# Optimization experiments

Measured on AMD Instinct MI355X. Metric: run time of the kernel, lower is better.

Reference implementation:

```python
import jax, jax.numpy as jnp
import numpy as np

B, L, H, NH, E, M, P, NL, BLK = 4, 1024, 768, 12, 24, 4, 552, 97, 64
NEG = -1e30

def setup_inputs() -> dict:
    key = jax.random.key(0)
    ks = jax.random.split(key, 10)
    sequence_output = jax.random.normal(ks[0], (B, L, H), jnp.float32)
    attention = jax.nn.softmax(jax.random.normal(ks[1], (B, NH, L, L), jnp.float32), axis=-1)
    mention_idx = jax.random.randint(ks[2], (B, E, M), 0, L)
    # first mention of each entity always valid, rest random (ragged mention counts)
    mention_mask = jnp.concatenate(
        [jnp.ones((B, E, 1), jnp.float32),
         (jax.random.uniform(ks[3], (B, E, M - 1)) > 0.4).astype(jnp.float32)], axis=-1)
    hts = jax.random.randint(ks[4], (B, P, 2), 0, E)
    s = 0.02
    Wh = jax.random.normal(ks[5], (H, 2 * H), jnp.float32) * s
    bh = jnp.zeros((H,), jnp.float32)
    Wt = jax.random.normal(ks[6], (H, 2 * H), jnp.float32) * s
    bt = jnp.zeros((H,), jnp.float32)
    Wb = jax.random.normal(ks[7], (NL, H * BLK), jnp.float32) * s
    bb = jnp.zeros((NL,), jnp.float32)
    return {"sequence_output": sequence_output, "attention": attention,
            "mention_mask": mention_mask, "Wh": Wh, "bh": bh, "Wt": Wt, "bt": bt,
            "Wb": Wb, "bb": bb, "mention_idx": mention_idx, "hts": hts}

def reference(sequence_output, attention, mention_mask, Wh, bh, Wt, bt, Wb, bb, mention_idx, hts):
    bix = jnp.arange(B)[:, None, None]
    # gather mention embeddings: [B,E,M,H]
    m_emb = sequence_output[bix, mention_idx]
    mask = mention_mask[..., None]
    # entity embedding: logsumexp over valid mentions
    entity_embs = jax.nn.logsumexp(jnp.where(mask > 0, m_emb, NEG), axis=2)  # [B,E,H]
    # gather mention attention rows: [B,E,M,NH,L]; mean over valid mentions
    m_att = attention[bix, :, mention_idx]
    denom = jnp.sum(mention_mask, axis=-1)[:, :, None, None]
    entity_atts = jnp.sum(m_att * mask[..., None], axis=2) / denom  # [B,E,NH,L]
    b2 = jnp.arange(B)[:, None]
    hs = entity_embs[b2, hts[..., 0]]   # [B,P,H]
    ts = entity_embs[b2, hts[..., 1]]
    h_att = entity_atts[b2, hts[..., 0]]  # [B,P,NH,L]
    t_att = entity_atts[b2, hts[..., 1]]
    ht_att = (h_att * t_att).mean(axis=2)                     # [B,P,L]
    ht_att = ht_att / (ht_att.sum(-1, keepdims=True) + 1e-5)
    rs = jnp.einsum('bld,brl->brd', sequence_output, ht_att)  # [B,P,H]
    zh = jnp.tanh(jnp.concatenate([hs, rs], -1) @ Wh.T + bh)  # [B,P,H]
    zt = jnp.tanh(jnp.concatenate([ts, rs], -1) @ Wt.T + bt)
    b1 = zh.reshape(B, P, H // BLK, BLK)
    b2_ = zt.reshape(B, P, H // BLK, BLK)
    bl = (b1[..., :, None] * b2_[..., None, :]).reshape(B, P, H * BLK)
    logits = bl @ Wb.T + bb                                   # [B,P,NL]
    return logits
```

## Files before the change

### kernel.cpp

```cpp
#include <hip/hip_runtime.h>
#include <math.h>

#define B_   4
#define L_   1024
#define H_   768
#define NH_  12
#define E_   24
#define M_   4
#define P_   552
#define NL_  97
#define H2_  1536
#define HB_  49152
#define R_   2208
#define NEG_ (-1e30f)

#define RT2_  9
#define PR2_  2304
#define S_    24
#define NTIL_ 7
#define KT_   1536

typedef _Float16 h2   __attribute__((ext_vector_type(2)));
typedef _Float16 f16x8 __attribute__((ext_vector_type(8)));
typedef float    f32x4 __attribute__((ext_vector_type(4)));

__device__ inline uint pkh(float lo, float hi) {
    union { __fp16 v __attribute__((ext_vector_type(2))); uint u; } c;
    c.v = __builtin_amdgcn_cvt_pkrtz(lo, hi);
    return c.u;
}
__device__ inline ushort h_rne(float x) {
    union { _Float16 h; ushort u; } c; c.h = (_Float16)x; return c.u;
}
__device__ inline uint h2_rne(float lo, float hi) {
    return (uint)h_rne(lo) | ((uint)h_rne(hi) << 16);
}

#define PKB_ATT 1152
#define PKB_WB  2688
#define PKB_W   576
#define PKB_SEQ 1536
#define PKB_EMB 96
__global__ void k_pack(const float* __restrict__ att, const float* __restrict__ Wb,
                       const float* __restrict__ Wh, const float* __restrict__ Wt,
                       const float* __restrict__ seq,
                       const int* __restrict__ midx, const float* __restrict__ mmask,
                       _Float16* __restrict__ ea, _Float16* __restrict__ WbP,
                       _Float16* __restrict__ WhP, _Float16* __restrict__ WtP,
                       _Float16* __restrict__ seqP, _Float16* __restrict__ ee) {
    int bid = blockIdx.x;
    if (bid < PKB_ATT) {
        int blk = bid;
        int n  = blk % NH_;
        int be = blk / NH_;
        int b  = be / E_;
        int idx[M_]; float msk[M_]; float denom = 0.f;
#pragma unroll
        for (int m = 0; m < M_; ++m) { idx[m] = midx[be*M_+m]; msk[m] = mmask[be*M_+m]; denom += msk[m]; }
        float inv = 1.f / denom;
        const float* abase = att + (size_t)(b*NH_ + n) * L_ * L_;
        int l4 = threadIdx.x * 4;
        float s0 = 0.f, s1 = 0.f, s2 = 0.f, s3 = 0.f;
#pragma unroll
        for (int m = 0; m < M_; ++m) {
            float4 a = *(const float4*)(abase + idx[m]*L_ + l4);
            s0 += msk[m]*a.x; s1 += msk[m]*a.y; s2 += msk[m]*a.z; s3 += msk[m]*a.w;
        }
        *(uint2*)(ea + (((size_t)(be*NH_ + n)) << 10) + l4) =
            make_uint2(pkh(s0*inv, s1*inv), pkh(s2*inv, s3*inv));
        return;
    }
    if (bid < PKB_ATT + PKB_WB) {
        int t = (bid - PKB_ATT)*256 + threadIdx.x;
        int lane = t & 63;
        int nt   = (t >> 6) % NTIL_;
        int kt   = t / (NTIL_*64);
        int n = nt*16 + (lane & 15);
        int k = kt*32 + ((lane >> 4) << 3);
        uint w[4] = {0u,0u,0u,0u};
        if (n < NL_) {
            const float* src = Wb + (size_t)n*HB_ + k;
#pragma unroll
            for (int e = 0; e < 4; ++e) w[e] = h2_rne(src[2*e], src[2*e+1]);
        }
        *(uint4*)(WbP + (size_t)t*8) = make_uint4(w[0],w[1],w[2],w[3]);
        return;
    }
    if (bid < PKB_ATT + PKB_WB + 2*PKB_W) {
        int seg = bid - PKB_ATT - PKB_WB;
        const float* W = (seg < PKB_W) ? Wh : Wt;
        _Float16*   WP = (seg < PKB_W) ? WhP : WtP;
        int t = (seg % PKB_W)*256 + threadIdx.x;
        int lane = t & 63;
        int nt   = (t >> 6) % 48;
        int kt   = t / (48*64);
        int n = nt*16 + (lane & 15);
        int k = kt*32 + ((lane >> 4) << 3);
        const float* src = W + (size_t)n*H2_ + k;
        uint w[4];
#pragma unroll
        for (int e = 0; e < 4; ++e) w[e] = h2_rne(src[2*e], src[2*e+1]);
        *(uint4*)(WP + (size_t)t*8) = make_uint4(w[0],w[1],w[2],w[3]);
        return;
    }
    if (bid < PKB_ATT + PKB_WB + 2*PKB_W + PKB_SEQ) {
        int t = (bid - PKB_ATT - PKB_WB - 2*PKB_W)*256 + threadIdx.x;
        int lane = t & 63;
        int rest = t >> 6;
        int nt = rest % 48; rest /= 48;
        int kt = rest % 32;
        int b  = rest / 32;
        int n = nt*16 + (lane & 15);
        int k = kt*32 + ((lane >> 4) << 3);
        const float* src = seq + ((size_t)(b*L_ + k))*H_ + n;
        uint w[4];
#pragma unroll
        for (int e = 0; e < 4; ++e) w[e] = h2_rne(src[(2*e)*H_], src[(2*e+1)*H_]);
        *(uint4*)(seqP + (size_t)t*8) = make_uint4(w[0],w[1],w[2],w[3]);
        return;
    }
    int be = bid - (PKB_ATT + PKB_WB + 2*PKB_W + PKB_SEQ);
    int b  = be / E_;
    int idx[M_]; float msk[M_];
#pragma unroll
    for (int m = 0; m < M_; ++m) { idx[m] = midx[be*M_+m]; msk[m] = mmask[be*M_+m]; }
    for (int d = threadIdx.x; d < H_; d += 256) {
        float v[M_]; float mx = NEG_;
#pragma unroll
        for (int m = 0; m < M_; ++m) {
            v[m] = (msk[m] > 0.f) ? seq[(b*L_ + idx[m])*H_ + d] : NEG_;
            mx = fmaxf(mx, v[m]);
        }
        float s = 0.f;
#pragma unroll
        for (int m = 0; m < M_; ++m) s += expf(v[m] - mx);
        ee[be*H_ + d] = (_Float16)(mx + logf(s));
    }
}

__global__ void k_ht_att(const _Float16* __restrict__ ea, const int* __restrict__ hts,
                         _Float16* __restrict__ ht) {
    __shared__ float red[2];
    int bp = blockIdx.x;
    int b  = bp / P_;
    int h = hts[bp*2+0], t = hts[bp*2+1];
    const uint4* eh4 = (const uint4*)(ea + ((size_t)(b*E_ + h)*NH_ << 10));
    const uint4* et4 = (const uint4*)(ea + ((size_t)(b*E_ + t)*NH_ << 10));
    int lp = threadIdx.x;
    float s[8] = {};
#pragma unroll
    for (int n = 0; n < NH_; ++n) {
        union { uint4 u; h2 v[4]; } A, C;
        A.u = eh4[n*128 + lp];
        C.u = et4[n*128 + lp];
#pragma unroll
        for (int q = 0; q < 4; ++q) {
            s[2*q]   += (float)A.v[q][0]*(float)C.v[q][0];
            s[2*q+1] += (float)A.v[q][1]*(float)C.v[q][1];
        }
    }
    float local = 0.f;
#pragma unroll
    for (int q = 0; q < 8; ++q) { s[q] *= (1.f/NH_); local += s[q]; }
#pragma unroll
    for (int o = 32; o > 0; o >>= 1) local += __shfl_down(local, o);
    int wid = threadIdx.x >> 6, lane = threadIdx.x & 63;
    if (lane == 0) red[wid] = local;
    __syncthreads();
    if (threadIdx.x == 0) red[0] = 1.f / (red[0] + red[1] + 1e-5f);
    __syncthreads();
    float inv = red[0];
    *(uint4*)(ht + ((size_t)bp << 10) + lp*8) =
        make_uint4(pkh(s[0]*inv, s[1]*inv), pkh(s[2]*inv, s[3]*inv),
                   pkh(s[4]*inv, s[5]*inv), pkh(s[6]*inv, s[7]*inv));
}

__launch_bounds__(256, 4)
__global__ void k_rs_mfma(const _Float16* __restrict__ ht, const _Float16* __restrict__ seqP,
                          _Float16* __restrict__ rs) {
    __shared__ _Float16 as[64*72];
    int bid = blockIdx.x;
    int xcd = bid & 7, j = bid >> 3;
    int b    = xcd >> 1;
    int tile = (xcd & 1)*54 + j;
    int p0   = (tile % 9) * 64;
    int nt0  = (tile / 9) * 4;
    int wave = threadIdx.x >> 6, lane = threadIdx.x & 63;

    const _Float16* srcp[2];
    int ldst[2];
#pragma unroll
    for (int i = 0; i < 2; ++i) {
        int t = threadIdx.x + i*256;
        int row = t >> 3, c8 = (t & 7)*8;
        int p = p0 + row;
        srcp[i] = (p < P_) ? ht + (((size_t)(b*P_ + p)) << 10) + c8 : nullptr;
        ldst[i] = row*72 + c8;
    }
    uint4 st[2];
#pragma unroll
    for (int i = 0; i < 2; ++i)
        st[i] = srcp[i] ? *(const uint4*)(srcp[i]) : make_uint4(0,0,0,0);

    f32x4 acc[4] = {};
    const _Float16* wbase = seqP + ((size_t)b*32*48 + nt0)*512 + lane*8;
    int rowA = wave*16 + (lane & 15);
    int asub = (lane >> 4) << 3;

    for (int kc = 0; kc < 16; ++kc) {
        if (kc) __syncthreads();
#pragma unroll
        for (int i = 0; i < 2; ++i) *(uint4*)(as + ldst[i]) = st[i];
        __syncthreads();
        if (kc + 1 < 16) {
#pragma unroll
            for (int i = 0; i < 2; ++i)
                st[i] = srcp[i] ? *(const uint4*)(srcp[i] + (kc+1)*64) : make_uint4(0,0,0,0);
        }
#pragma unroll
        for (int kk = 0; kk < 2; ++kk) {
            int kt = kc*2 + kk;
            const _Float16* wp = wbase + (size_t)kt*(48*512);
            f16x8 bf[4];
#pragma unroll
            for (int jj = 0; jj < 4; ++jj) bf[jj] = *(const f16x8*)(wp + jj*512);
            f16x8 af = *(const f16x8*)(as + rowA*72 + kk*32 + asub);
#pragma unroll
            for (int jj = 0; jj < 4; ++jj)
                acc[jj] = __builtin_amdgcn_mfma_f32_16x16x32_f16(af, bf[jj], acc[jj], 0, 0, 0);
        }
    }
    int crow = (lane >> 4) * 4;
    int ccol = lane & 15;
#pragma unroll
    for (int jj = 0; jj < 4; ++jj) {
        int n = nt0*16 + jj*16 + ccol;
#pragma unroll
        for (int reg = 0; reg < 4; ++reg) {
            int p = p0 + wave*16 + crow + reg;
            if (p < P_) rs[(size_t)(b*P_ + p)*H_ + n] = (_Float16)acc[jj][reg];
        }
    }
}

__launch_bounds__(256, 4)
__global__ void k_z_mfma(const _Float16* __restrict__ ee, const _Float16* __restrict__ rs,
                         const _Float16* __restrict__ WhP, const _Float16* __restrict__ WtP,
                         const float* __restrict__ bh, const float* __restrict__ bt,
                         const int* __restrict__ hts,
                         _Float16* __restrict__ zh, _Float16* __restrict__ zt) {
    __shared__ _Float16 as[64*72];
    int bid = blockIdx.x;
    int xcd = bid & 7, j = bid >> 3;
    int which = xcd >> 2;
    int tile  = (xcd & 3)*105 + j;
    int r0  = (tile % 35) * 64;
    int nt0 = (tile / 35) * 4;
    const _Float16* WP   = which ? WtP : WhP;
    const float*    bias = which ? bt  : bh;
    _Float16*       out  = which ? zt  : zh;
    int wave = threadIdx.x >> 6, lane = threadIdx.x & 63;

    const _Float16* srcA[2];
    const _Float16* srcB[2];
    int ldst[2];
#pragma unroll
    for (int i = 0; i < 2; ++i) {
        int t = threadIdx.x + i*256;
        int row = t >> 3, c8 = (t & 7)*8;
        int r = r0 + row;
        if (r < R_) {
            int b = r / P_;
            int eidx = hts[r*2 + which];
            srcA[i] = ee + (size_t)(b*E_ + eidx)*H_ + c8;
            srcB[i] = rs + (size_t)r*H_ + c8;
        } else { srcA[i] = nullptr; srcB[i] = nullptr; }
        ldst[i] = row*72 + c8;
    }
    uint4 st[2];
#pragma unroll
    for (int i = 0; i < 2; ++i)
        st[i] = srcA[i] ? *(const uint4*)(srcA[i]) : make_uint4(0,0,0,0);

    f32x4 acc[4] = {};
    const _Float16* wbase = WP + (size_t)nt0*512 + lane*8;
    int rowA = wave*16 + (lane & 15);
    int asub = (lane >> 4) << 3;

    for (int kc = 0; kc < 24; ++kc) {
        if (kc) __syncthreads();
#pragma unroll
        for (int i = 0; i < 2; ++i) *(uint4*)(as + ldst[i]) = st[i];
        __syncthreads();
        if (kc + 1 < 24) {
            int kn = kc + 1;
#pragma unroll
            for (int i = 0; i < 2; ++i) {
                const _Float16* s = (kn < 12) ? (srcA[i] ? srcA[i] + kn*64 : nullptr)
                                              : (srcB[i] ? srcB[i] + (kn-12)*64 : nullptr);
                st[i] = s ? *(const uint4*)s : make_uint4(0,0,0,0);
            }
        }
#pragma unroll
        for (int kk = 0; kk < 2; ++kk) {
            int kt = kc*2 + kk;
            const _Float16* wp = wbase + (size_t)kt*(48*512);
            f16x8 bf[4];
#pragma unroll
            for (int jj = 0; jj < 4; ++jj) bf[jj] = *(const f16x8*)(wp + jj*512);
            f16x8 af = *(const f16x8*)(as + rowA*72 + kk*32 + asub);
#pragma unroll
            for (int jj = 0; jj < 4; ++jj)
                acc[jj] = __builtin_amdgcn_mfma_f32_16x16x32_f16(af, bf[jj], acc[jj], 0, 0, 0);
        }
    }
    int crow = (lane >> 4) * 4;
    int ccol = lane & 15;
#pragma unroll
    for (int jj = 0; jj < 4; ++jj) {
        int n = nt0*16 + jj*16 + ccol;
        float bv = bias[n];
#pragma unroll
        for (int reg = 0; reg < 4; ++reg) {
            int r = r0 + wave*16 + crow + reg;
            if (r < R_) out[(size_t)r*H_ + n] = (_Float16)tanhf(acc[jj][reg] + bv);
        }
    }
}

__launch_bounds__(512, 2)
__global__ void k_logits_mfma(const _Float16* __restrict__ zh, const _Float16* __restrict__ zt,
                              const _Float16* __restrict__ WbP, float* __restrict__ part) {
    __shared__ _Float16 zhs[256*40];
    __shared__ _Float16 zts[256*72];
    int bid = blockIdx.x;
    int xcd = bid & 7, j = bid >> 3;
    int kc  = xcd*3 + j/9;
    int rt  = j % 9;
    int r0  = rt * 256;
    int kblk = kc >> 1, i0 = (kc & 1) * 32;

    for (int t = threadIdx.x; t < 256*4; t += 512) {
        int row = t >> 2, i8 = (t & 3)*8;
        int r = r0 + row;
        uint4 w = make_uint4(0,0,0,0);
        if (r < R_) w = *(const uint4*)(zh + (size_t)r*H_ + kblk*64 + i0 + i8);
        *(uint4*)(zhs + row*40 + i8) = w;
    }
    for (int t = threadIdx.x; t < 256*8; t += 512) {
        int row = t >> 3, j8 = (t & 7)*8;
        int r = r0 + row;
        uint4 w = make_uint4(0,0,0,0);
        if (r < R_) w = *(const uint4*)(zt + (size_t)r*H_ + kblk*64 + j8);
        *(uint4*)(zts + row*72 + j8) = w;
    }
    __syncthreads();

    int wave = threadIdx.x >> 6, lane = threadIdx.x & 63;
    int rowA0 = wave*32 + (lane & 15);
    int jsub  = (lane >> 4) * 8;

    f32x4 acc[2][NTIL_] = {};
    const _Float16* wb0 = WbP + (size_t)(kc*64) * (NTIL_*512) + lane*8;

    f16x8 bf[NTIL_];
#pragma unroll
    for (int nt = 0; nt < NTIL_; ++nt) bf[nt] = *(const f16x8*)(wb0 + nt*512);

    for (int ktl = 0; ktl < 64; ++ktl) {
        f16x8 bn[NTIL_];
        if (ktl + 1 < 64) {
            const _Float16* wp = wb0 + (size_t)(ktl+1) * (NTIL_*512);
#pragma unroll
            for (int nt = 0; nt < NTIL_; ++nt) bn[nt] = *(const f16x8*)(wp + nt*512);
        }
        int il = ktl >> 1;
        int jb = (ktl & 1) * 32 + jsub;
#pragma unroll
        for (int ms = 0; ms < 2; ++ms) {
            int row = rowA0 + ms*16;
            _Float16 hv = zhs[row*40 + il];
            h2 hb = {hv, hv};
            union { uint4 u; h2 v[4]; } T;
            T.u = *(const uint4*)(zts + row*72 + jb);
            union { h2 v[4]; f16x8 f; } A;
            A.v[0] = hb * T.v[0];
            A.v[1] = hb * T.v[1];
            A.v[2] = hb * T.v[2];
            A.v[3] = hb * T.v[3];
#pragma unroll
            for (int nt = 0; nt < NTIL_; ++nt)
                acc[ms][nt] = __builtin_amdgcn_mfma_f32_16x16x32_f16(A.f, bf[nt], acc[ms][nt], 0, 0, 0);
        }
        if (ktl + 1 < 64) {
#pragma unroll
            for (int nt = 0; nt < NTIL_; ++nt) bf[nt] = bn[nt];
        }
    }

    int crow0 = wave*32 + (lane >> 4) * 4;
    int ccol  = lane & 15;
#pragma unroll
    for (int ms = 0; ms < 2; ++ms) {
#pragma unroll
        for (int nt = 0; nt < NTIL_; ++nt) {
#pragma unroll
            for (int reg = 0; reg < 4; ++reg) {
                int rp = r0 + crow0 + ms*16 + reg;
                part[((size_t)kc*PR2_ + rp)*112 + nt*16 + ccol] = acc[ms][nt][reg];
            }
        }
    }
}

__global__ void k_logits_reduce(const float* __restrict__ part, const float* __restrict__ bb,
                                float* __restrict__ out) {
    int idx = blockIdx.x*256 + threadIdx.x;
    if (idx >= R_*NL_) return;
    int r = idx / NL_, n = idx - r*NL_;
    float s = bb[n];
#pragma unroll
    for (int kc = 0; kc < S_; ++kc) s += part[((size_t)kc*PR2_ + r)*112 + n];
    out[idx] = s;
}

extern "C" void kernel_launch(void* const* d_in, const int* in_sizes, int n_in,
                              void* d_out, int out_size, void* d_ws, size_t ws_size,
                              hipStream_t stream) {
    const float* seq   = (const float*)d_in[0];
    const float* att   = (const float*)d_in[1];
    const float* mmask = (const float*)d_in[2];
    const float* Wh    = (const float*)d_in[3];
    const float* bh    = (const float*)d_in[4];
    const float* Wt    = (const float*)d_in[5];
    const float* bt    = (const float*)d_in[6];
    const float* Wb    = (const float*)d_in[7];
    const float* bb    = (const float*)d_in[8];
    const int*   midx  = (const int*)d_in[9];
    const int*   hts   = (const int*)d_in[10];
    float* out = (float*)d_out;

    char* base = (char*)d_ws;
    _Float16* WbP  = (_Float16*)base;  base += (size_t)KT_*NTIL_*64*8 * 2;
    _Float16* WhP  = (_Float16*)base;  base += (size_t)48*48*64*8 * 2;
    _Float16* WtP  = (_Float16*)base;  base += (size_t)48*48*64*8 * 2;
    _Float16* seqP = (_Float16*)base;  base += (size_t)B_*32*48*64*8 * 2;
    _Float16* ee   = (_Float16*)base;  base += (size_t)B_*E_*H_ * 2;
    _Float16* ea   = (_Float16*)base;  base += (size_t)B_*E_*NH_*L_ * 2;
    _Float16* ht   = (_Float16*)base;  base += (size_t)R_*L_ * 2;
    _Float16* rs   = (_Float16*)base;  base += (size_t)R_*H_ * 2;
    _Float16* zh   = (_Float16*)base;  base += (size_t)R_*H_ * 2;
    _Float16* zt   = (_Float16*)base;  base += (size_t)R_*H_ * 2;
    float*    part = (float*)base;

    k_pack<<<dim3(PKB_ATT + PKB_WB + 2*PKB_W + PKB_SEQ + PKB_EMB), dim3(256), 0, stream>>>(
        att, Wb, Wh, Wt, seq, midx, mmask, ea, WbP, WhP, WtP, seqP, ee);

    k_ht_att<<<dim3(R_), dim3(128), 0, stream>>>(ea, hts, ht);

    k_rs_mfma<<<dim3(432), dim3(256), 0, stream>>>(ht, seqP, rs);

    k_z_mfma<<<dim3(840), dim3(256), 0, stream>>>(ee, rs, WhP, WtP, bh, bt, hts, zh, zt);

    k_logits_mfma  <<<dim3(216), dim3(512), 0, stream>>>(zh, zt, WbP, part);
    k_logits_reduce<<<dim3((R_*NL_ + 255)/256), dim3(256), 0, stream>>>(part, bb, out);
}
```

Before: 122.8 us.

## Enlarge GEMM row tiles to 128 and split logits K finer with fp16 partials

The rs and z GEMM kernels now compute 128-row tiles per block, with each wave handling two 16-row MFMA subtiles. Each weight fragment loaded from global memory is therefore reused twice, and fewer blocks are launched. The logits kernel splits the K dimension into 48 chunks instead of 24, uses 256-thread blocks with 64 rows per wave, and writes its partial sums in fp16 instead of fp32. This cuts partial-buffer traffic but adds fp16 rounding to each partial sum and lowers occupancy through larger register tiles.

```diff
diff --git a/kernel.cpp b/kernel.cpp
--- a/kernel.cpp
+++ b/kernel.cpp
@@ -16,7 +16,7 @@
 
 #define RT2_  9
 #define PR2_  2304
-#define S_    24
+#define S_    48
 #define NTIL_ 7
 #define KT_   1536
 
@@ -175,46 +175,46 @@
                    pkh(s[4]*inv, s[5]*inv), pkh(s[6]*inv, s[7]*inv));
 }
 
-__launch_bounds__(256, 4)
+__launch_bounds__(256, 2)
 __global__ void k_rs_mfma(const _Float16* __restrict__ ht, const _Float16* __restrict__ seqP,
                           _Float16* __restrict__ rs) {
-    __shared__ _Float16 as[64*72];
+    __shared__ _Float16 as[128*72];
     int bid = blockIdx.x;
-    int xcd = bid & 7, j = bid >> 3;
+    int xcd = bid & 7, jj0 = bid >> 3;
     int b    = xcd >> 1;
-    int tile = (xcd & 1)*54 + j;
-    int p0   = (tile % 9) * 64;
-    int nt0  = (tile / 9) * 4;
+    int tile = (xcd & 1)*30 + jj0;
+    int p0   = (tile % 5) * 128;
+    int nt0  = (tile / 5) * 4;
     int wave = threadIdx.x >> 6, lane = threadIdx.x & 63;
 
-    const _Float16* srcp[2];
-    int ldst[2];
-#pragma unroll
-    for (int i = 0; i < 2; ++i) {
+    const _Float16* srcp[4];
+    int ldst[4];
+#pragma unroll
+    for (int i = 0; i < 4; ++i) {
         int t = threadIdx.x + i*256;
         int row = t >> 3, c8 = (t & 7)*8;
         int p = p0 + row;
         srcp[i] = (p < P_) ? ht + (((size_t)(b*P_ + p)) << 10) + c8 : nullptr;
         ldst[i] = row*72 + c8;
     }
-    uint4 st[2];
-#pragma unroll
-    for (int i = 0; i < 2; ++i)
+    uint4 st[4];
+#pragma unroll
+    for (int i = 0; i < 4; ++i)
         st[i] = srcp[i] ? *(const uint4*)(srcp[i]) : make_uint4(0,0,0,0);
 
-    f32x4 acc[4] = {};
+    f32x4 acc[2][4] = {};
     const _Float16* wbase = seqP + ((size_t)b*32*48 + nt0)*512 + lane*8;
-    int rowA = wave*16 + (lane & 15);
+    int rowbase = wave*32 + (lane & 15);
     int asub = (lane >> 4) << 3;
 
     for (int kc = 0; kc < 16; ++kc) {
         if (kc) __syncthreads();
 #pragma unroll
-        for (int i = 0; i < 2; ++i) *(uint4*)(as + ldst[i]) = st[i];
+        for (int i = 0; i < 4; ++i) *(uint4*)(as + ldst[i]) = st[i];
         __syncthreads();
         if (kc + 1 < 16) {
 #pragma unroll
-            for (int i = 0; i < 2; ++i)
+            for (int i = 0; i < 4; ++i)
                 st[i] = srcp[i] ? *(const uint4*)(srcp[i] + (kc+1)*64) : make_uint4(0,0,0,0);
         }
 #pragma unroll
@@ -223,49 +223,55 @@
             const _Float16* wp = wbase + (size_t)kt*(48*512);
             f16x8 bf[4];
 #pragma unroll
-            for (int jj = 0; jj < 4; ++jj) bf[jj] = *(const f16x8*)(wp + jj*512);
-            f16x8 af = *(const f16x8*)(as + rowA*72 + kk*32 + asub);
-#pragma unroll
-            for (int jj = 0; jj < 4; ++jj)
-                acc[jj] = __builtin_amdgcn_mfma_f32_16x16x32_f16(af, bf[jj], acc[jj], 0, 0, 0);
+            for (int jn = 0; jn < 4; ++jn) bf[jn] = *(const f16x8*)(wp + jn*512);
+#pragma unroll
+            for (int ms = 0; ms < 2; ++ms) {
+                f16x8 af = *(const f16x8*)(as + (rowbase + ms*16)*72 + kk*32 + asub);
+#pragma unroll
+                for (int jn = 0; jn < 4; ++jn)
+                    acc[ms][jn] = __builtin_amdgcn_mfma_f32_16x16x32_f16(af, bf[jn], acc[ms][jn], 0, 0, 0);
+            }
         }
     }
     int crow = (lane >> 4) * 4;
     int ccol = lane & 15;
 #pragma unroll
-    for (int jj = 0; jj < 4; ++jj) {
-        int n = nt0*16 + jj*16 + ccol;
-#pragma unroll
-        for (int reg = 0; reg < 4; ++reg) {
-            int p = p0 + wave*16 + crow + reg;
-            if (p < P_) rs[(size_t)(b*P_ + p)*H_ + n] = (_Float16)acc[jj][reg];
-        }
-    }
-}
-
-__launch_bounds__(256, 4)
+    for (int ms = 0; ms < 2; ++ms) {
+#pragma unroll
+        for (int jn = 0; jn < 4; ++jn) {
+            int n = nt0*16 + jn*16 + ccol;
+#pragma unroll
+            for (int reg = 0; reg < 4; ++reg) {
+                int p = p0 + wave*32 + ms*16 + crow + reg;
+                if (p < P_) rs[(size_t)(b*P_ + p)*H_ + n] = (_Float16)acc[ms][jn][reg];
+            }
+        }
+    }
+}
+
+__launch_bounds__(256, 2)
 __global__ void k_z_mfma(const _Float16* __restrict__ ee, const _Float16* __restrict__ rs,
                          const _Float16* __restrict__ WhP, const _Float16* __restrict__ WtP,
                          const float* __restrict__ bh, const float* __restrict__ bt,
                          const int* __restrict__ hts,
                          _Float16* __restrict__ zh, _Float16* __restrict__ zt) {
-    __shared__ _Float16 as[64*72];
+    __shared__ _Float16 as[128*72];
     int bid = blockIdx.x;
-    int xcd = bid & 7, j = bid >> 3;
+    int xcd = bid & 7, jj0 = bid >> 3;
     int which = xcd >> 2;
-    int tile  = (xcd & 3)*105 + j;
-    int r0  = (tile % 35) * 64;
-    int nt0 = (tile / 35) * 4;
+    int tile  = (xcd & 3)*54 + jj0;
+    int r0  = (tile % 18) * 128;
+    int nt0 = (tile / 18) * 4;
     const _Float16* WP   = which ? WtP : WhP;
     const float*    bias = which ? bt  : bh;
     _Float16*       out  = which ? zt  : zh;
     int wave = threadIdx.x >> 6, lane = threadIdx.x & 63;
 
-    const _Float16* srcA[2];
-    const _Float16* srcB[2];
-    int ldst[2];
-#pragma unroll
-    for (int i = 0; i < 2; ++i) {
+    const _Float16* srcA[4];
+    const _Float16* srcB[4];
+    int ldst[4];
+#pragma unroll
+    for (int i = 0; i < 4; ++i) {
         int t = threadIdx.x + i*256;
         int row = t >> 3, c8 = (t & 7)*8;
         int r = r0 + row;
@@ -277,25 +283,25 @@
         } else { srcA[i] = nullptr; srcB[i] = nullptr; }
         ldst[i] = row*72 + c8;
     }
-    uint4 st[2];
-#pragma unroll
-    for (int i = 0; i < 2; ++i)
+    uint4 st[4];
+#pragma unroll
+    for (int i = 0; i < 4; ++i)
         st[i] = srcA[i] ? *(const uint4*)(srcA[i]) : make_uint4(0,0,0,0);
 
-    f32x4 acc[4] = {};
+    f32x4 acc[2][4] = {};
     const _Float16* wbase = WP + (size_t)nt0*512 + lane*8;
-    int rowA = wave*16 + (lane & 15);
+    int rowbase = wave*32 + (lane & 15);
     int asub = (lane >> 4) << 3;
 
     for (int kc = 0; kc < 24; ++kc) {
         if (kc) __syncthreads();
 #pragma unroll
-        for (int i = 0; i < 2; ++i) *(uint4*)(as + ldst[i]) = st[i];
+        for (int i = 0; i < 4; ++i) *(uint4*)(as + ldst[i]) = st[i];
         __syncthreads();
         if (kc + 1 < 24) {
             int kn = kc + 1;
 #pragma unroll
-            for (int i = 0; i < 2; ++i) {
+            for (int i = 0; i < 4; ++i) {
                 const _Float16* s = (kn < 12) ? (srcA[i] ? srcA[i] + kn*64 : nullptr)
                                               : (srcB[i] ? srcB[i] + (kn-12)*64 : nullptr);
                 st[i] = s ? *(const uint4*)s : make_uint4(0,0,0,0);
@@ -307,69 +313,78 @@
             const _Float16* wp = wbase + (size_t)kt*(48*512);
             f16x8 bf[4];
 #pragma unroll
-            for (int jj = 0; jj < 4; ++jj) bf[jj] = *(const f16x8*)(wp + jj*512);
-            f16x8 af = *(const f16x8*)(as + rowA*72 + kk*32 + asub);
-#pragma unroll
-            for (int jj = 0; jj < 4; ++jj)
-                acc[jj] = __builtin_amdgcn_mfma_f32_16x16x32_f16(af, bf[jj], acc[jj], 0, 0, 0);
+            for (int jn = 0; jn < 4; ++jn) bf[jn] = *(const f16x8*)(wp + jn*512);
+#pragma unroll
+            for (int ms = 0; ms < 2; ++ms) {
+                f16x8 af = *(const f16x8*)(as + (rowbase + ms*16)*72 + kk*32 + asub);
+#pragma unroll
+                for (int jn = 0; jn < 4; ++jn)
+                    acc[ms][jn] = __builtin_amdgcn_mfma_f32_16x16x32_f16(af, bf[jn], acc[ms][jn], 0, 0, 0);
+            }
         }
     }
     int crow = (lane >> 4) * 4;
     int ccol = lane & 15;
 #pragma unroll
-    for (int jj = 0; jj < 4; ++jj) {
-        int n = nt0*16 + jj*16 + ccol;
-        float bv = bias[n];
-#pragma unroll
-        for (int reg = 0; reg < 4; ++reg) {
-            int r = r0 + wave*16 + crow + reg;
-            if (r < R_) out[(size_t)r*H_ + n] = (_Float16)tanhf(acc[jj][reg] + bv);
-        }
-    }
-}
-
-__launch_bounds__(512, 2)
+    for (int ms = 0; ms < 2; ++ms) {
+#pragma unroll
+        for (int jn = 0; jn < 4; ++jn) {
+            int n = nt0*16 + jn*16 + ccol;
+            float bv = bias[n];
+#pragma unroll
+            for (int reg = 0; reg < 4; ++reg) {
+                int r = r0 + wave*32 + ms*16 + crow + reg;
+                if (r < R_) out[(size_t)r*H_ + n] = (_Float16)tanhf(acc[ms][jn][reg] + bv);
+            }
+        }
+    }
+}
+
+__launch_bounds__(256, 2)
 __global__ void k_logits_mfma(const _Float16* __restrict__ zh, const _Float16* __restrict__ zt,
-                              const _Float16* __restrict__ WbP, float* __restrict__ part) {
-    __shared__ _Float16 zhs[256*40];
+                              const _Float16* __restrict__ WbP, _Float16* __restrict__ part) {
+    __shared__ _Float16 zhs[256*20];
     __shared__ _Float16 zts[256*72];
     int bid = blockIdx.x;
     int xcd = bid & 7, j = bid >> 3;
-    int kc  = xcd*3 + j/9;
+    int kc  = xcd*6 + j/9;
     int rt  = j % 9;
     int r0  = rt * 256;
-    int kblk = kc >> 1, i0 = (kc & 1) * 32;
-
-    for (int t = threadIdx.x; t < 256*4; t += 512) {
-        int row = t >> 2, i8 = (t & 3)*8;
+    int g64 = (kc >> 2) * 64;
+    int a0  = (kc & 3) * 16;
+
+    for (int it = 0; it < 2; ++it) {
+        int t = threadIdx.x + it*256;
+        int row = t >> 1, i8 = (t & 1)*8;
         int r = r0 + row;
         uint4 w = make_uint4(0,0,0,0);
-        if (r < R_) w = *(const uint4*)(zh + (size_t)r*H_ + kblk*64 + i0 + i8);
-        *(uint4*)(zhs + row*40 + i8) = w;
-    }
-    for (int t = threadIdx.x; t < 256*8; t += 512) {
+        if (r < R_) w = *(const uint4*)(zh + (size_t)r*H_ + g64 + a0 + i8);
+        *(uint4*)(zhs + row*20 + i8) = w;
+    }
+    for (int it = 0; it < 8; ++it) {
+        int t = threadIdx.x + it*256;
         int row = t >> 3, j8 = (t & 7)*8;
         int r = r0 + row;
         uint4 w = make_uint4(0,0,0,0);
-        if (r < R_) w = *(const uint4*)(zt + (size_t)r*H_ + kblk*64 + j8);
+        if (r < R_) w = *(const uint4*)(zt + (size_t)r*H_ + g64 + j8);
         *(uint4*)(zts + row*72 + j8) = w;
     }
     __syncthreads();
 
     int wave = threadIdx.x >> 6, lane = threadIdx.x & 63;
-    int rowA0 = wave*32 + (lane & 15);
+    int rowA0 = wave*64 + (lane & 15);
     int jsub  = (lane >> 4) * 8;
 
-    f32x4 acc[2][NTIL_] = {};
-    const _Float16* wb0 = WbP + (size_t)(kc*64) * (NTIL_*512) + lane*8;
+    f32x4 acc[4][NTIL_] = {};
+    const _Float16* wb0 = WbP + (size_t)(kc*32) * (NTIL_*512) + lane*8;
 
     f16x8 bf[NTIL_];
 #pragma unroll
     for (int nt = 0; nt < NTIL_; ++nt) bf[nt] = *(const f16x8*)(wb0 + nt*512);
 
-    for (int ktl = 0; ktl < 64; ++ktl) {
+    for (int ktl = 0; ktl < 32; ++ktl) {
         f16x8 bn[NTIL_];
-        if (ktl + 1 < 64) {
+        if (ktl + 1 < 32) {
             const _Float16* wp = wb0 + (size_t)(ktl+1) * (NTIL_*512);
 #pragma unroll
             for (int nt = 0; nt < NTIL_; ++nt) bn[nt] = *(const f16x8*)(wp + nt*512);
@@ -377,9 +392,9 @@
         int il = ktl >> 1;
         int jb = (ktl & 1) * 32 + jsub;
 #pragma unroll
-        for (int ms = 0; ms < 2; ++ms) {
+        for (int ms = 0; ms < 4; ++ms) {
             int row = rowA0 + ms*16;
-            _Float16 hv = zhs[row*40 + il];
+            _Float16 hv = zhs[row*20 + il];
             h2 hb = {hv, hv};
             union { uint4 u; h2 v[4]; } T;
             T.u = *(const uint4*)(zts + row*72 + jb);
@@ -392,35 +407,35 @@
             for (int nt = 0; nt < NTIL_; ++nt)
                 acc[ms][nt] = __builtin_amdgcn_mfma_f32_16x16x32_f16(A.f, bf[nt], acc[ms][nt], 0, 0, 0);
         }
-        if (ktl + 1 < 64) {
+        if (ktl + 1 < 32) {
 #pragma unroll
             for (int nt = 0; nt < NTIL_; ++nt) bf[nt] = bn[nt];
         }
     }
 
-    int crow0 = wave*32 + (lane >> 4) * 4;
+    int crow0 = wave*64 + (lane >> 4) * 4;
     int ccol  = lane & 15;
 #pragma unroll
-    for (int ms = 0; ms < 2; ++ms) {
+    for (int ms = 0; ms < 4; ++ms) {
 #pragma unroll
         for (int nt = 0; nt < NTIL_; ++nt) {
 #pragma unroll
             for (int reg = 0; reg < 4; ++reg) {
                 int rp = r0 + crow0 + ms*16 + reg;
-                part[((size_t)kc*PR2_ + rp)*112 + nt*16 + ccol] = acc[ms][nt][reg];
-            }
-        }
-    }
-}
-
-__global__ void k_logits_reduce(const float* __restrict__ part, const float* __restrict__ bb,
+                part[((size_t)kc*PR2_ + rp)*112 + nt*16 + ccol] = (_Float16)acc[ms][nt][reg];
+            }
+        }
+    }
+}
+
+__global__ void k_logits_reduce(const _Float16* __restrict__ part, const float* __restrict__ bb,
                                 float* __restrict__ out) {
     int idx = blockIdx.x*256 + threadIdx.x;
     if (idx >= R_*NL_) return;
     int r = idx / NL_, n = idx - r*NL_;
     float s = bb[n];
 #pragma unroll
-    for (int kc = 0; kc < S_; ++kc) s += part[((size_t)kc*PR2_ + r)*112 + n];
+    for (int kc = 0; kc < S_; ++kc) s += (float)part[((size_t)kc*PR2_ + r)*112 + n];
     out[idx] = s;
 }
 
@@ -451,17 +466,17 @@
     _Float16* rs   = (_Float16*)base;  base += (size_t)R_*H_ * 2;
     _Float16* zh   = (_Float16*)base;  base += (size_t)R_*H_ * 2;
     _Float16* zt   = (_Float16*)base;  base += (size_t)R_*H_ * 2;
-    float*    part = (float*)base;
+    _Float16* part = (_Float16*)base;
 
     k_pack<<<dim3(PKB_ATT + PKB_WB + 2*PKB_W + PKB_SEQ + PKB_EMB), dim3(256), 0, stream>>>(
         att, Wb, Wh, Wt, seq, midx, mmask, ea, WbP, WhP, WtP, seqP, ee);
 
     k_ht_att<<<dim3(R_), dim3(128), 0, stream>>>(ea, hts, ht);
 
-    k_rs_mfma<<<dim3(432), dim3(256), 0, stream>>>(ht, seqP, rs);
-
-    k_z_mfma<<<dim3(840), dim3(256), 0, stream>>>(ee, rs, WhP, WtP, bh, bt, hts, zh, zt);
-
-    k_logits_mfma  <<<dim3(216), dim3(512), 0, stream>>>(zh, zt, WbP, part);
+    k_rs_mfma<<<dim3(240), dim3(256), 0, stream>>>(ht, seqP, rs);
+
+    k_z_mfma<<<dim3(432), dim3(256), 0, stream>>>(ee, rs, WhP, WtP, bh, bt, hts, zh, zt);
+
+    k_logits_mfma  <<<dim3(432), dim3(256), 0, stream>>>(zh, zt, WbP, part);
     k_logits_reduce<<<dim3((R_*NL_ + 255)/256), dim3(256), 0, stream>>>(part, bb, out);
 }
```

Result: faster. 114.6 us (-6.7%).
